# Kernel optimization log

Measured on AMD Instinct MI355X. Metric: run time of the kernel, lower is better.

Reference implementation:

```python
import jax, jax.numpy as jnp
import numpy as np

K = 3           # spatial kernel size (kernel_size[1]==kernel_size[2])
STRIDE = 1
EPS_BN = 1e-5


def unfold_replicate(t, k=K, stride=STRIDE):
    """t: (b, C, H, W) -> (b, C, k*k, H//stride, W//stride).
    Replicate-padded kxk patches, row-major window order (matches F.pad(replicate)+F.unfold)."""
    b, C, H, W = t.shape
    pad = (k - 1) // 2
    tp = jnp.pad(t, ((0, 0), (0, 0), (pad, pad), (pad, pad)), mode='edge')
    patches = [tp[:, :, di:di + H:stride, dj:dj + W:stride]
               for di in range(k) for dj in range(k)]
    return jnp.stack(patches, axis=2)


def grid_sample_3d(x, grid):
    """Trilinear grid sample, zeros padding, align_corners=True.
    x: (b,c,D,H,W); grid: (b,P,3) normalized (gx,gy,gz) -> (b,c,P)."""
    b, c, D, H, W = x.shape
    ix = (grid[..., 0] + 1.0) * 0.5 * (W - 1)
    iy = (grid[..., 1] + 1.0) * 0.5 * (H - 1)
    iz = (grid[..., 2] + 1.0) * 0.5 * (D - 1)
    x0 = jnp.floor(ix); y0 = jnp.floor(iy); z0 = jnp.floor(iz)
    fx = ix - x0; fy = iy - y0; fz = iz - z0
    x0i = x0.astype(jnp.int32); y0i = y0.astype(jnp.int32); z0i = z0.astype(jnp.int32)
    x_flat = x.reshape(b, c, D * H * W)
    gather = jax.vmap(lambda xf, idx: xf[:, idx])  # (c,N),(P) -> (c,P) per batch
    out = jnp.zeros((b, c, ix.shape[1]), dtype=x.dtype)
    for dz, wz in ((0, 1.0 - fz), (1, fz)):
        zi = z0i + dz
        for dy, wy in ((0, 1.0 - fy), (1, fy)):
            yi = y0i + dy
            for dx, wx in ((0, 1.0 - fx), (1, fx)):
                xi = x0i + dx
                valid = ((zi >= 0) & (zi < D) & (yi >= 0) & (yi < H)
                         & (xi >= 0) & (xi < W))
                idx = (jnp.clip(zi, 0, D - 1) * H + jnp.clip(yi, 0, H - 1)) * W \
                      + jnp.clip(xi, 0, W - 1)
                w = (wz * wy * wx) * valid.astype(x.dtype)
                out = out + w[:, None, :] * gather(x_flat, idx)
    return out


def gca_cost(x, dp, normal, intri):
    b, c, d, H, W = x.shape
    k2 = K * K
    h, w = H // STRIDE, W // STRIDE
    ctr = k2 // 2

    dp_unf = unfold_replicate(dp)        # (b, d, k2, h, w)
    n_unf = unfold_replicate(normal)     # (b, 3, k2, h, w)
    nx, ny, nz = n_unf[:, 0], n_unf[:, 1], n_unf[:, 2]

    fx = intri[:, 0, 0][:, None, None]; fy = intri[:, 1, 1][:, None, None]
    cx = intri[:, 0, 2][:, None, None]; cy = intri[:, 1, 2][:, None, None]
    yg, xg = jnp.meshgrid(jnp.arange(H, dtype=x.dtype),
                          jnp.arange(W, dtype=x.dtype), indexing='ij')
    posx = (xg[None] - cx) / fx          # (b, H, W) normalized camera rays
    posy = (yg[None] - cy) / fy
    pos_unf = unfold_replicate(jnp.stack([posx, posy], axis=1))  # (b,2,k2,h,w)
    pu, pv = pos_unf[:, 0], pos_unf[:, 1]
    pu_c = pu[:, ctr:ctr + 1]; pv_c = pv[:, ctr:ctr + 1]

    num = nx * pu_c + ny * pv_c + nz
    den = nx * pu + ny * pv + nz
    den = jnp.where(jnp.abs(den) < 1e-8, jnp.sign(den) * 1e-8, den)
    wgt = num / den
    wgt = jnp.where(jnp.isfinite(wgt), wgt, 1.0)   # (b, k2, h, w)

    dp_ctr = dp_unf[:, :, ctr]                      # (b, d, h, w)
    dp_prog = wgt[:, None] * dp_ctr[:, :, None]     # (b, d, k2, h, w)
    interval = dp_unf[:, 1] - dp_unf[:, 0]          # (b, k2, h, w)
    z = (dp_prog - dp_unf[:, 0][:, None]) / interval[:, None]  # (b,d,k2,h,w)

    xy = jnp.broadcast_to(jnp.stack([xg, yg], axis=0)[None], (b, 2, H, W))
    xy_unf = unfold_replicate(xy)                   # (b,2,k2,h,w)
    px = jnp.broadcast_to(xy_unf[:, 0][:, None], (b, d, k2, h, w))
    py = jnp.broadcast_to(xy_unf[:, 1][:, None], (b, d, k2, h, w))

    gx = px / ((W - 1) / 2.0) - 1.0
    gy = py / ((H - 1) / 2.0) - 1.0
    gz = z / ((d - 1) / 2.0) - 1.0
    grid = jnp.stack([gx, gy, gz], axis=-1).reshape(b, d * k2 * h * w, 3)

    samp = grid_sample_3d(x, grid)                  # (b, c, d*k2*h*w)
    samp = samp.reshape(b, c, d, k2, h, w).transpose(0, 1, 3, 2, 4, 5)
    return samp.reshape(b, c * k2, d, h, w)


def reference(x, dp, normal, intri, weight, gamma, beta):
    cost = gca_cost(x, dp, normal, intri)
    y = jax.lax.conv_general_dilated(
        cost, weight, window_strides=(1, 1, 1),
        padding=[(1, 1), (0, 0), (0, 0)],
        dimension_numbers=('NCDHW', 'OIDHW', 'NCDHW'))
    # BatchNorm3d (training-mode batch stats, biased var, eps=1e-5) + ReLU
    mean = jnp.mean(y, axis=(0, 2, 3, 4), keepdims=True)
    var = jnp.var(y, axis=(0, 2, 3, 4), keepdims=True)
    g = gamma.reshape(1, -1, 1, 1, 1)
    bta = beta.reshape(1, -1, 1, 1, 1)
    return jax.nn.relu(g * (y - mean) * jax.lax.rsqrt(var + EPS_BN) + bta)


def setup_inputs() -> dict:
    key = jax.random.key(0)
    ks = jax.random.split(key, 6)
    b, c, d, H, W = 1, 8, 32, 128, 128
    out_ch = 16
    x = jax.random.normal(ks[0], (b, c, d, H, W), dtype=jnp.float32)
    # monotone depth hypotheses per pixel (interval = dp[:,1]-dp[:,0] must be nonzero)
    planes = 425.0 + 10.0 * jnp.arange(d, dtype=jnp.float32)
    scale = 1.0 + 0.05 * jax.random.uniform(ks[1], (b, 1, H, W), dtype=jnp.float32)
    dp = planes[None, :, None, None] * scale                    # (b, d, H, W)
    # near-frontal unit normals so plane-homography weights stay well-conditioned
    nxy = 0.2 * jax.random.normal(ks[2], (b, 2, H, W), dtype=jnp.float32)
    nz = 1.0 + 0.1 * jax.random.normal(ks[3], (b, 1, H, W), dtype=jnp.float32)
    n = jnp.concatenate([nxy, nz], axis=1)
    normal = n / jnp.linalg.norm(n, axis=1, keepdims=True)
    intri = jnp.broadcast_to(
        jnp.array([[1100.0, 0.0, W / 2.0],
                   [0.0, 1100.0, H / 2.0],
                   [0.0, 0.0, 1.0]], dtype=jnp.float32), (b, 3, 3))
    weight = 0.05 * jax.random.normal(ks[4], (out_ch, c * K * K, 3, 1, 1),
                                      dtype=jnp.float32)
    gamma = jnp.ones((out_ch,), jnp.float32)
    beta = jnp.zeros((out_ch,), jnp.float32)
    return {"x": x, "dp": dp, "normal": normal, "intri": intri,
            "weight": weight, "gamma": gamma, "beta": beta}
```

## Files before the change

### kernel.cpp

```cpp
#include <hip/hip_runtime.h>
#include <math.h>

#define W_    128
#define H_    128
#define HW    16384
#define D_    32
#define C_IN  8
#define OC    16
#define NRED  524288.0f

#define SXS   36
#define SXB   1948
#define TILE  2568

typedef __attribute__((ext_vector_type(8))) short bf16x8;
typedef __attribute__((ext_vector_type(4))) float f32x4;

union FragU { uint4 u; bf16x8 h; };


__device__ __forceinline__ unsigned bf16rne(float f) {
    unsigned u = __float_as_uint(f);
    return (u + 0x7fffu + ((u >> 16) & 1u)) >> 16;
}

__global__ __launch_bounds__(256) void k_init(const float* __restrict__ wsrc,
                                              float* __restrict__ ws) {
    int t = threadIdx.x;
    if (t < 32) ws[t] = 0.f;
    uint4* af = reinterpret_cast<uint4*>(ws + 64);
    for (int e = t; e < 768; e += 256) {
        int lane = e & 63, pkd = e >> 6;
        int p = pkd / 3, kd = pkd - p * 3;
        int o = lane & 15, kg = lane >> 4;
        int ch = 2 * p + (kg >> 1);
        int jb = (kg & 1) * 8;
        unsigned dw[4];
#pragma unroll
        for (int r2 = 0; r2 < 4; ++r2) {
            int j0 = jb + 2 * r2, j1 = j0 + 1;
            unsigned b0 = (j0 < 9) ? bf16rne(wsrc[(o * 72 + ch * 9 + j0) * 3 + kd]) : 0u;
            unsigned b1 = (j1 < 9) ? bf16rne(wsrc[(o * 72 + ch * 9 + j1) * 3 + kd]) : 0u;
            dw[r2] = b0 | (b1 << 16);
        }
        af[e] = make_uint4(dw[0], dw[1], dw[2], dw[3]);
    }
}

template <bool YBF>
__global__ __launch_bounds__(512, 4) void k_main(const float* __restrict__ x,
                                                 const float* __restrict__ dp,
                                                 const float* __restrict__ nrm,
                                                 const float* __restrict__ intri,
                                                 const uint4* __restrict__ afr,
                                                 float* __restrict__ out,
                                                 unsigned* __restrict__ ybf,
                                                 float* __restrict__ stats) {
    __shared__ float s_pool[2 * SXB];
    __shared__ float s_B[2 * TILE];
    __shared__ float s_wgt[144], s_dp0[144], s_inv[144];
    __shared__ float s_red[64];

    int t   = threadIdx.x;
    int bid = blockIdx.x;
    int r_row = bid >> 3;
    int rx0   = (bid & 7) * 16;

    int seg = t / 144;
    int f   = t - seg * 144;
    int spx = f >> 3;
    int zq  = f & 7;
    int srow = min(max(r_row + seg - 1, 0), H_ - 1);
    int scol = min(max(rx0 - 1 + spx, 0), W_ - 1);
    const float* gsrc_raw = x + (srow * W_ + scol) + (size_t)(zq * 4) * HW;
    int sdst = 4 + (seg * 18 + spx) * SXS + zq * 4;

    float4 sv;
    if (t < 432) {
        sv.x = gsrc_raw[0]; sv.y = gsrc_raw[HW];
        sv.z = gsrc_raw[2 * HW]; sv.w = gsrc_raw[3 * HW];
    }

    if (t < 144) {
        int p = t / 9, j = t - p * 9;
        int jd = j / 3;
        int dy = jd - 1, dx = (j - jd * 3) - 1;
        int cpix = rx0 + p;
        int ry  = min(max(r_row + dy, 0), H_ - 1);
        int rxn = min(max(cpix + dx, 0), W_ - 1);
        int nb  = ry * W_ + rxn;
        float fx = intri[0], cx = intri[2], fy = intri[4], cy = intri[5];
        float nx = nrm[nb], ny = nrm[HW + nb], nz = nrm[2 * HW + nb];
        float pu  = ((float)rxn  - cx) / fx;
        float pv  = ((float)ry   - cy) / fy;
        float puc = ((float)cpix - cx) / fx;
        float pvc = ((float)r_row - cy) / fy;
        float num = nx * puc + ny * pvc + nz;
        float den = nx * pu + ny * pv + nz;
        if (fabsf(den) < 1e-8f)
            den = (den > 0.f) ? 1e-8f : ((den < 0.f) ? -1e-8f : 0.f);
        float w = num / den;
        if (!isfinite(w)) w = 1.0f;
        float d0  = dp[nb];
        float itv = dp[HW + nb] - d0;
        s_wgt[t] = w;
        s_dp0[t] = d0;
        s_inv[t] = 1.0f / itv;
    }
    if (t < 440) {
        int b  = t / 220;
        int rm = t - b * 220;
        int off = (rm < 4) ? rm : (4 + ((rm - 4) >> 2) * SXS + 32 + ((rm - 4) & 3));
        s_pool[b * SXB + off] = 0.f;
    }
    if (t < 16) s_B[2560 + (t >> 3) * TILE + (t & 7)] = 0.f;
    __syncthreads();
    if (t < 432) *reinterpret_cast<float4*>(&s_pool[sdst]) = sv;

    int px = t & 15;
    int d  = t >> 4;
    float dpv = dp[d * HW + r_row * W_ + rx0 + px];

    int   idx[9];
    float fza[9];
#pragma unroll
    for (int j = 0; j < 9; ++j) {
        int pj = px * 9 + j;
        int jd = j / 3;
        int jx = j - jd * 3;
        float z   = (s_wgt[pj] * dpv - s_dp0[pj]) * s_inv[pj];
        float zc  = fminf(fmaxf(z, -2.0f), 34.0f);
        float z0f = floorf(zc);
        fza[j] = zc - z0f;
        idx[j] = (jd * 18 + px + jx) * SXS + (int)z0f;
    }
    __syncthreads();

    f32x4 acc0 = {0.f, 0.f, 0.f, 0.f};
    f32x4 acc1 = {0.f, 0.f, 0.f, 0.f};
    f32x4 acc2 = {0.f, 0.f, 0.f, 0.f};
    f32x4 acc3 = {0.f, 0.f, 0.f, 0.f};

    int lane = t & 63;
    int wid  = t >> 6;
    int wb   = wid * 4;
    int grp  = lane >> 4;
    unsigned* sBu = reinterpret_cast<unsigned*>(s_B);
    int wrow = (d * 16 + px) * 5;

    for (int c = 0; c < C_IN; ++c) {
        if (c < 7 && t < 432) {
            const float* b = gsrc_raw + (size_t)(c + 1) * (D_ * HW);
            sv.x = b[0]; sv.y = b[HW]; sv.z = b[2 * HW]; sv.w = b[3 * HW];
        }
        const float* sxp = &s_pool[(c & 1) * SXB + 4];
        float cj[9];
#pragma unroll
        for (int j = 0; j < 9; ++j) {
            float a = sxp[idx[j]];
            float b = sxp[idx[j] + 1];
            cj[j] = fmaf(fza[j], b - a, a);
        }
        unsigned dwv[5];
#pragma unroll
        for (int r2 = 0; r2 < 4; ++r2) {
            asm("v_cvt_pk_bf16_f32 %0, %1, %2"
                : "=v"(dwv[r2]) : "v"(cj[2 * r2]), "v"(cj[2 * r2 + 1]));
        }
        {
            float zz = 0.f;
            asm("v_cvt_pk_bf16_f32 %0, %1, %2"
                : "=v"(dwv[4]) : "v"(cj[8]), "v"(zz));
        }
        {
            int wo = wrow + (c & 1) * TILE;
            sBu[wo + 0] = dwv[0];
            sBu[wo + 1] = dwv[1];
            sBu[wo + 2] = dwv[2];
            sBu[wo + 3] = dwv[3];
            sBu[wo + 4] = dwv[4];
        }
        if (c < 7 && t < 432) *reinterpret_cast<float4*>(&s_pool[((c + 1) & 1) * SXB + sdst]) = sv;
        __syncthreads();

        if (c & 1) {
            int p = c >> 1;
            FragU a0, a1, a2;
            a0.u = afr[(p * 3 + 0) * 64 + lane];
            a1.u = afr[(p * 3 + 1) * 64 + lane];
            a2.u = afr[(p * 3 + 2) * 64 + lane];
            int boff = ((grp & 1) ? 4 : 0) + ((grp >> 1) ? TILE : 0);
#pragma unroll
            for (int q = 0; q < 6; ++q) {
                int db = wb - 1 + q;
                if (db < 0 || db > 31) continue;
                FragU bf;
                int base = (db * 16 + px) * 5 + boff;
                bf.u.x = sBu[base + 0];
                bf.u.y = sBu[base + 1];
                bf.u.z = sBu[base + 2];
                bf.u.w = sBu[base + 3];
                if (q - 0 >= 0 && q - 0 < 4)
                    *(q == 0 ? &acc0 : q == 1 ? &acc1 : q == 2 ? &acc2 : &acc3) =
                        __builtin_amdgcn_mfma_f32_16x16x32_bf16(a0.h, bf.h,
                            *(q == 0 ? &acc0 : q == 1 ? &acc1 : q == 2 ? &acc2 : &acc3), 0, 0, 0);
                if (q - 1 >= 0 && q - 1 < 4)
                    *(q == 1 ? &acc0 : q == 2 ? &acc1 : q == 3 ? &acc2 : &acc3) =
                        __builtin_amdgcn_mfma_f32_16x16x32_bf16(a1.h, bf.h,
                            *(q == 1 ? &acc0 : q == 2 ? &acc1 : q == 3 ? &acc2 : &acc3), 0, 0, 0);
                if (q - 2 >= 0 && q - 2 < 4)
                    *(q == 2 ? &acc0 : q == 3 ? &acc1 : q == 4 ? &acc2 : &acc3) =
                        __builtin_amdgcn_mfma_f32_16x16x32_bf16(a2.h, bf.h,
                            *(q == 2 ? &acc0 : q == 3 ? &acc1 : q == 4 ? &acc2 : &acc3), 0, 0, 0);
            }
            __syncthreads();
        }
    }

    float* s_b = s_pool;
    float bns[4], bnq[4];
    int o_l = t >> 7;
    int dd  = (t >> 2) & 31;
    int q4  = t & 3;
#pragma unroll
    for (int oo = 0; oo < 4; ++oo) {
        if (grp == oo) {
#pragma unroll
            for (int r2 = 0; r2 < 4; ++r2) {
                s_b[(r2 * 32 + wb + 0) * 17 + px] = acc0[r2];
                s_b[(r2 * 32 + wb + 1) * 17 + px] = acc1[r2];
                s_b[(r2 * 32 + wb + 2) * 17 + px] = acc2[r2];
                s_b[(r2 * 32 + wb + 3) * 17 + px] = acc3[r2];
            }
        }
        __syncthreads();
        const float* brow = &s_b[(o_l * 32 + dd) * 17 + q4 * 4];
        float4 yv;
        yv.x = brow[0]; yv.y = brow[1]; yv.z = brow[2]; yv.w = brow[3];
        int o = oo * 4 + o_l;
        size_t base = (size_t)(o * 32 + dd) * HW + r_row * W_ + rx0 + q4 * 4;
        if (YBF) {
            unsigned dA, dB;
            asm("v_cvt_pk_bf16_f32 %0, %1, %2" : "=v"(dA) : "v"(yv.x), "v"(yv.y));
            asm("v_cvt_pk_bf16_f32 %0, %1, %2" : "=v"(dB) : "v"(yv.z), "v"(yv.w));
            uint2 wv; wv.x = dA; wv.y = dB;
            reinterpret_cast<uint2*>(ybf)[base >> 2] = wv;
        } else {
            *reinterpret_cast<float4*>(out + base) = yv;
        }
        bns[oo] = yv.x + yv.y + yv.z + yv.w;
        bnq[oo] = yv.x * yv.x + yv.y * yv.y + yv.z * yv.z + yv.w * yv.w;
        __syncthreads();
    }

#pragma unroll
    for (int oo = 0; oo < 4; ++oo) {
        float s = bns[oo], sq = bnq[oo];
#pragma unroll
        for (int m = 1; m < 64; m <<= 1) {
            s  += __shfl_xor(s, m, 64);
            sq += __shfl_xor(sq, m, 64);
        }
        if ((t & 63) == 0) {
            int w = t >> 6;
            s_red[w * 4 + oo]      = s;
            s_red[32 + w * 4 + oo] = sq;
        }
    }
    __syncthreads();
    if (t < 32) {
        int o  = t & 15;
        int oo = o >> 2, wh = o & 3;
        if (t < 16) {
            float s = s_red[(2 * wh) * 4 + oo] + s_red[(2 * wh + 1) * 4 + oo];
            atomicAdd(&stats[o], s);
        } else {
            float sq = s_red[32 + (2 * wh) * 4 + oo] + s_red[32 + (2 * wh + 1) * 4 + oo];
            atomicAdd(&stats[16 + o], sq);
        }
    }
}

template <bool YBF>
__global__ __launch_bounds__(256) void k_bn(float* __restrict__ out,
                                            const unsigned* __restrict__ ybf,
                                            const float* __restrict__ stats,
                                            const float* __restrict__ gamma,
                                            const float* __restrict__ beta) {
    int i4 = blockIdx.x * 256 + threadIdx.x;
    int o  = i4 >> 17;
    float invN = 1.f / NRED;
    float mean = stats[o] * invN;
    float var  = stats[16 + o] * invN - mean * mean;
    float rstd = rsqrtf(var + 1e-5f);
    float a = gamma[o] * rstd;
    float b = beta[o] - mean * a;
    float4 y;
    if (YBF) {
        uint2 v = reinterpret_cast<const uint2*>(ybf)[i4];
        y.x = __uint_as_float(v.x << 16);
        y.y = __uint_as_float(v.x & 0xffff0000u);
        y.z = __uint_as_float(v.y << 16);
        y.w = __uint_as_float(v.y & 0xffff0000u);
    } else {
        y = reinterpret_cast<float4*>(out)[i4];
    }
    y.x = fmaxf(0.f, fmaf(y.x, a, b));
    y.y = fmaxf(0.f, fmaf(y.y, a, b));
    y.z = fmaxf(0.f, fmaf(y.z, a, b));
    y.w = fmaxf(0.f, fmaf(y.w, a, b));
    reinterpret_cast<float4*>(out)[i4] = y;
}

extern "C" void kernel_launch(void* const* d_in, const int* in_sizes, int n_in,
                              void* d_out, int out_size, void* d_ws, size_t ws_size,
                              hipStream_t stream) {
    const float* x     = (const float*)d_in[0];
    const float* dp    = (const float*)d_in[1];
    const float* nrm   = (const float*)d_in[2];
    const float* intri = (const float*)d_in[3];
    const float* wsrc  = (const float*)d_in[4];
    const float* gamma = (const float*)d_in[5];
    const float* beta  = (const float*)d_in[6];
    float* out = (float*)d_out;
    float* ws  = (float*)d_ws;

    bool yb_ok = ws_size >= (size_t)(8192 + 4194304) * 4;
    unsigned* ybf = (unsigned*)(ws + 8192);
    const uint4* afr = (const uint4*)(ws + 64);

    hipLaunchKernelGGL(k_init, dim3(1), dim3(256), 0, stream, wsrc, ws);
    if (yb_ok) {
        hipLaunchKernelGGL(k_main<true>, dim3(1024), dim3(512), 0, stream,
                           x, dp, nrm, intri, afr, out, ybf, ws);
        hipLaunchKernelGGL(k_bn<true>, dim3(8192), dim3(256), 0, stream,
                           out, ybf, ws, gamma, beta);
    } else {
        hipLaunchKernelGGL(k_main<false>, dim3(1024), dim3(512), 0, stream,
                           x, dp, nrm, intri, afr, out, ybf, ws);
        hipLaunchKernelGGL(k_bn<false>, dim3(8192), dim3(256), 0, stream,
                           out, ybf, ws, gamma, beta);
    }
}
```

Baseline: 59.06 us.

## Store x pool as packed bf16 neighbor pairs for single-load z interpolation

Changes the shared x staging buffer from fp32 depth columns to packed bf16 pairs (z, z+1) per word, so each trilinear tap needs one LDS load instead of two. Each thread now loads five global values (one overlapping) and packs them, adding global loads and conversion work. It also rounds x to bf16 before interpolation, which adds precision loss, and moves the epilogue scratch buffer to s_B.

```diff
diff --git a/kernel.cpp b/kernel.cpp
--- a/kernel.cpp
+++ b/kernel.cpp
@@ -9,8 +9,8 @@
 #define OC    16
 #define NRED  524288.0f
 
-#define SXS   36
-#define SXB   1948
+#define SXS2  37
+#define SXB2  1998
 #define TILE  2568
 
 typedef __attribute__((ext_vector_type(8))) short bf16x8;
@@ -56,7 +56,7 @@
                                                  float* __restrict__ out,
                                                  unsigned* __restrict__ ybf,
                                                  float* __restrict__ stats) {
-    __shared__ float s_pool[2 * SXB];
+    __shared__ unsigned s_poolU[2 * SXB2];
     __shared__ float s_B[2 * TILE];
     __shared__ float s_wgt[144], s_dp0[144], s_inv[144];
     __shared__ float s_red[64];
@@ -72,13 +72,17 @@
     int zq  = f & 7;
     int srow = min(max(r_row + seg - 1, 0), H_ - 1);
     int scol = min(max(rx0 - 1 + spx, 0), W_ - 1);
-    const float* gsrc_raw = x + (srow * W_ + scol) + (size_t)(zq * 4) * HW;
-    int sdst = 4 + (seg * 18 + spx) * SXS + zq * 4;
-
-    float4 sv;
+    const float* gsrc_raw = x + (srow * W_ + scol);
+    int colL = seg * 18 + spx;
+    int sdst = colL * SXS2 + 1 + 4 * zq;
+
+    float xv[5];
     if (t < 432) {
-        sv.x = gsrc_raw[0]; sv.y = gsrc_raw[HW];
-        sv.z = gsrc_raw[2 * HW]; sv.w = gsrc_raw[3 * HW];
+#pragma unroll
+        for (int i = 0; i < 5; ++i) {
+            int z = 4 * zq - 1 + i;
+            xv[i] = (z >= 0) ? gsrc_raw[(size_t)z * HW] : 0.f;
+        }
     }
 
     if (t < 144) {
@@ -107,21 +111,39 @@
         s_dp0[t] = d0;
         s_inv[t] = 1.0f / itv;
     }
-    if (t < 440) {
-        int b  = t / 220;
-        int rm = t - b * 220;
-        int off = (rm < 4) ? rm : (4 + ((rm - 4) >> 2) * SXS + 32 + ((rm - 4) & 3));
-        s_pool[b * SXB + off] = 0.f;
+    if (t < 432) {
+        int b  = t / 216;
+        int rm = t - b * 216;
+        int col = rm >> 2, w4 = rm & 3;
+        int off = col * SXS2 + ((w4 == 0) ? 0 : (33 + w4));
+        s_poolU[b * SXB2 + off] = 0u;
     }
     if (t < 16) s_B[2560 + (t >> 3) * TILE + (t & 7)] = 0.f;
     __syncthreads();
-    if (t < 432) *reinterpret_cast<float4*>(&s_pool[sdst]) = sv;
+    if (t < 432) {
+        unsigned pd[4];
+#pragma unroll
+        for (int i = 0; i < 4; ++i) {
+            asm("v_cvt_pk_bf16_f32 %0, %1, %2"
+                : "=v"(pd[i]) : "v"(xv[i]), "v"(xv[i + 1]));
+        }
+        s_poolU[sdst + 0] = pd[0];
+        s_poolU[sdst + 1] = pd[1];
+        s_poolU[sdst + 2] = pd[2];
+        s_poolU[sdst + 3] = pd[3];
+        if (zq == 7) {
+            unsigned pe;
+            float zz = 0.f;
+            asm("v_cvt_pk_bf16_f32 %0, %1, %2" : "=v"(pe) : "v"(xv[4]), "v"(zz));
+            s_poolU[colL * SXS2 + 33] = pe;
+        }
+    }
 
     int px = t & 15;
     int d  = t >> 4;
     float dpv = dp[d * HW + r_row * W_ + rx0 + px];
 
-    int   idx[9];
+    int   idq[9];
     float fza[9];
 #pragma unroll
     for (int j = 0; j < 9; ++j) {
@@ -132,7 +154,7 @@
         float zc  = fminf(fmaxf(z, -2.0f), 34.0f);
         float z0f = floorf(zc);
         fza[j] = zc - z0f;
-        idx[j] = (jd * 18 + px + jx) * SXS + (int)z0f;
+        idq[j] = (jd * 18 + px + jx) * SXS2 + 2 + (int)z0f;
     }
     __syncthreads();
 
@@ -150,15 +172,20 @@
 
     for (int c = 0; c < C_IN; ++c) {
         if (c < 7 && t < 432) {
-            const float* b = gsrc_raw + (size_t)(c + 1) * (D_ * HW);
-            sv.x = b[0]; sv.y = b[HW]; sv.z = b[2 * HW]; sv.w = b[3 * HW];
-        }
-        const float* sxp = &s_pool[(c & 1) * SXB + 4];
+            const float* bp = gsrc_raw + (size_t)(c + 1) * (D_ * HW);
+#pragma unroll
+            for (int i = 0; i < 5; ++i) {
+                int z = 4 * zq - 1 + i;
+                xv[i] = (z >= 0) ? bp[(size_t)z * HW] : 0.f;
+            }
+        }
+        const unsigned* PU = s_poolU + (c & 1) * SXB2;
         float cj[9];
 #pragma unroll
         for (int j = 0; j < 9; ++j) {
-            float a = sxp[idx[j]];
-            float b = sxp[idx[j] + 1];
+            unsigned u = PU[idq[j]];
+            float a = __uint_as_float(u << 16);
+            float b = __uint_as_float(u & 0xffff0000u);
             cj[j] = fmaf(fza[j], b - a, a);
         }
         unsigned dwv[5];
@@ -180,7 +207,25 @@
             sBu[wo + 3] = dwv[3];
             sBu[wo + 4] = dwv[4];
         }
-        if (c < 7 && t < 432) *reinterpret_cast<float4*>(&s_pool[((c + 1) & 1) * SXB + sdst]) = sv;
+        if (c < 7 && t < 432) {
+            int ds2 = ((c + 1) & 1) * SXB2;
+            unsigned pd[4];
+#pragma unroll
+            for (int i = 0; i < 4; ++i) {
+                asm("v_cvt_pk_bf16_f32 %0, %1, %2"
+                    : "=v"(pd[i]) : "v"(xv[i]), "v"(xv[i + 1]));
+            }
+            s_poolU[ds2 + sdst + 0] = pd[0];
+            s_poolU[ds2 + sdst + 1] = pd[1];
+            s_poolU[ds2 + sdst + 2] = pd[2];
+            s_poolU[ds2 + sdst + 3] = pd[3];
+            if (zq == 7) {
+                unsigned pe;
+                float zz = 0.f;
+                asm("v_cvt_pk_bf16_f32 %0, %1, %2" : "=v"(pe) : "v"(xv[4]), "v"(zz));
+                s_poolU[ds2 + colL * SXS2 + 33] = pe;
+            }
+        }
         __syncthreads();
 
         if (c & 1) {
@@ -217,7 +262,7 @@
         }
     }
 
-    float* s_b = s_pool;
+    float* s_b = s_B;
     float bns[4], bnq[4];
     int o_l = t >> 7;
     int dd  = (t >> 2) & 31;
```

New measurement: 62.24 us. 1.05x slower.
